# Performance work log

Measured on AMD Instinct MI355X. Metric: run time of the kernel, lower is better.

Reference implementation:

```python
import jax, jax.numpy as jnp
import numpy as np

C, H, W, B = 64, 64, 64, 8

def setup_inputs() -> dict:
    key = jax.random.key(0)
    ks = jax.random.split(key, 6)
    s = 0.05
    return {
        "x": jax.random.normal(ks[0], (B, C, H, W), dtype=jnp.float32),
        "w_cam": jax.random.normal(ks[1], (C, C), dtype=jnp.float32) * s,        # CAM 1x1 conv
        "w_q": jax.random.normal(ks[2], (C // 2, C), dtype=jnp.float32) * s,     # SAM query 1x1 conv
        "w_k": jax.random.normal(ks[3], (C // 2, C), dtype=jnp.float32) * s,     # SAM key 1x1 conv
        "w_v": jax.random.normal(ks[4], (C, C), dtype=jnp.float32) * s,          # SAM value 1x1 conv
        "w_bn": jax.random.normal(ks[5], (C, 2 * C), dtype=jnp.float32) * s,     # bottleneck 1x1 conv 2c->c
    }

def _conv1x1(w, x):
    # w: [O, C], x: [B, C, H, W] -> [B, O, H, W]
    return jnp.einsum('oc,bchw->bohw', w, x)

def reference(x, w_cam, w_q, w_k, w_v, w_bn):
    b, c, h, w = x.shape
    hw = h * w
    # ---- CAM (channel attention) ----
    xc = _conv1x1(w_cam, x).reshape(b, c, hw)            # [b, c, hw]
    energy_c = jnp.einsum('bcn,bdn->bcd', xc, xc)        # [b, c, c]
    attn_c = jax.nn.softmax(energy_c, axis=-1)           # dropout = identity (eval)
    out_c = jnp.einsum('bcd,bdn->bcn', attn_c, x.reshape(b, c, hw)).reshape(b, c, h, w)
    # ---- SAM (spatial attention) ----
    q = _conv1x1(w_q, x).reshape(b, c // 2, hw)          # [b, c/2, hw]
    k = _conv1x1(w_k, x).reshape(b, c // 2, hw)
    v = _conv1x1(w_v, x).reshape(b, c, hw)
    energy_s = jnp.einsum('bcn,bcm->bnm', q, k)          # [b, hw, hw]
    attn_s = jax.nn.softmax(energy_s, axis=-1)           # dropout = identity (eval)
    out_s = jnp.einsum('bcm,bnm->bcn', v, attn_s).reshape(b, c, h, w)
    # ---- fuse: concat -> bottleneck 1x1 conv -> residual ----
    cat = jnp.concatenate([out_c, out_s], axis=1)        # [b, 2c, h, w]
    out = _conv1x1(w_bn, cat)                            # [b, c, h, w]
    return x + out
```

## Files before the change

### kernel.cpp

```cpp
#include <hip/hip_runtime.h>

#define BB 8
#define C 64
#define HW 4096

typedef __attribute__((ext_vector_type(8))) __bf16 bf16x8;
typedef __attribute__((ext_vector_type(16))) float f32x16;
typedef unsigned int uint;
typedef unsigned short ushort;

__device__ __forceinline__ ushort bfb(float f) {
  return __builtin_bit_cast(ushort, (__bf16)f);
}
__device__ __forceinline__ uint pk2(float a, float b) {
  return (uint)bfb(a) | ((uint)bfb(b) << 16);
}
__device__ __forceinline__ uint cvtpk(float a, float b) {
  uint r;
  asm("v_cvt_pk_bf16_f32 %0, %1, %2" : "=v"(r) : "v"(a), "v"(b));
  return r;
}
__device__ __forceinline__ f32x16 mfma_bf16(bf16x8 a, bf16x8 b, f32x16 c) {
  return __builtin_amdgcn_mfma_f32_32x32x16_bf16(a, b, c, 0, 0, 0);
}

__global__ __launch_bounds__(256) void gram_fold_kernel(const float* __restrict__ x,
                                                        float* __restrict__ Gp,
                                                        const float* __restrict__ w_bn,
                                                        const float* __restrict__ w_q,
                                                        const float* __restrict__ w_k,
                                                        const float* __restrict__ w_v,
                                                        char* __restrict__ wall) {
  __shared__ float slots[4][4096];
  const int bxx = blockIdx.x;
  const int t = threadIdx.x;
  if (bxx < 4) {
    const int slot = bxx * 4 + (t >> 6);
    const int ot = slot >> 2, kc = slot & 3;
    const int l = t & 63, lo5 = l & 31, hi = l >> 5;
    float v[8];
    if (ot == 0) {
#pragma unroll
      for (int j = 0; j < 8; ++j)
        v[j] = 1.44269504088896f * w_q[lo5 * 64 + kc * 16 + hi * 8 + j];
    } else if (ot == 1) {
#pragma unroll
      for (int j = 0; j < 8; ++j) v[j] = w_k[lo5 * 64 + kc * 16 + hi * 8 + j];
    } else {
      int c = (ot - 2) * 32 + lo5;
#pragma unroll
      for (int j = 0; j < 8; ++j) {
        int d = kc * 16 + hi * 8 + j;
        float acc = 0.f;
        for (int e = 0; e < 64; ++e) acc += w_bn[c * 128 + 64 + e] * w_v[e * 64 + d];
        v[j] = acc;
      }
    }
    uint4 w;
    w.x = pk2(v[0], v[1]); w.y = pk2(v[2], v[3]);
    w.z = pk2(v[4], v[5]); w.w = pk2(v[6], v[7]);
    *(uint4*)(wall + slot * 1024 + l * 16) = w;
    return;
  }
  const int bx = bxx - 4;
  const int b = bx >> 3, kb = bx & 7;
  const int w = t >> 6, l = t & 63, lo5 = l & 31, hi = l >> 5;
  const int k0 = kb * 512 + w * 128;
  const float* xb = x + (size_t)b * C * HW;
  f32x16 fz;
#pragma unroll
  for (int r = 0; r < 16; ++r) fz[r] = 0.f;
  f32x16 a00 = fz, a01 = fz, a10 = fz, a11 = fz;
#pragma unroll 1
  for (int kc = 0; kc < 8; ++kc) {
    int nb = k0 + kc * 16 + hi * 8;
    const float4* p0 = (const float4*)(xb + (size_t)lo5 * HW + nb);
    const float4* p1 = (const float4*)(xb + (size_t)(32 + lo5) * HW + nb);
    float v0[8], v1[8];
    {
      float4 a = p0[0], bq = p0[1];
      v0[0] = a.x; v0[1] = a.y; v0[2] = a.z; v0[3] = a.w;
      v0[4] = bq.x; v0[5] = bq.y; v0[6] = bq.z; v0[7] = bq.w;
      float4 c = p1[0], d = p1[1];
      v1[0] = c.x; v1[1] = c.y; v1[2] = c.z; v1[3] = c.w;
      v1[4] = d.x; v1[5] = d.y; v1[6] = d.z; v1[7] = d.w;
    }
    uint4 uh0, ul0, uh1, ul1;
    {
      float h[8], e[8];
#pragma unroll
      for (int j = 0; j < 8; ++j) { h[j] = (float)(__bf16)v0[j]; e[j] = v0[j] - h[j]; }
      uh0.x = pk2(h[0], h[1]); uh0.y = pk2(h[2], h[3]); uh0.z = pk2(h[4], h[5]); uh0.w = pk2(h[6], h[7]);
      ul0.x = cvtpk(e[0], e[1]); ul0.y = cvtpk(e[2], e[3]); ul0.z = cvtpk(e[4], e[5]); ul0.w = cvtpk(e[6], e[7]);
#pragma unroll
      for (int j = 0; j < 8; ++j) { h[j] = (float)(__bf16)v1[j]; e[j] = v1[j] - h[j]; }
      uh1.x = pk2(h[0], h[1]); uh1.y = pk2(h[2], h[3]); uh1.z = pk2(h[4], h[5]); uh1.w = pk2(h[6], h[7]);
      ul1.x = cvtpk(e[0], e[1]); ul1.y = cvtpk(e[2], e[3]); ul1.z = cvtpk(e[4], e[5]); ul1.w = cvtpk(e[6], e[7]);
    }
    bf16x8 f0h = __builtin_bit_cast(bf16x8, uh0);
    bf16x8 f0l = __builtin_bit_cast(bf16x8, ul0);
    bf16x8 f1h = __builtin_bit_cast(bf16x8, uh1);
    bf16x8 f1l = __builtin_bit_cast(bf16x8, ul1);
    a00 = mfma_bf16(f0h, f0h, a00); a00 = mfma_bf16(f0h, f0l, a00); a00 = mfma_bf16(f0l, f0h, a00);
    a01 = mfma_bf16(f0h, f1h, a01); a01 = mfma_bf16(f0h, f1l, a01); a01 = mfma_bf16(f0l, f1h, a01);
    a10 = mfma_bf16(f1h, f0h, a10); a10 = mfma_bf16(f1h, f0l, a10); a10 = mfma_bf16(f1l, f0h, a10);
    a11 = mfma_bf16(f1h, f1h, a11); a11 = mfma_bf16(f1h, f1l, a11); a11 = mfma_bf16(f1l, f1h, a11);
  }
#pragma unroll
  for (int r = 0; r < 16; ++r) {
    int row = (r & 3) + 8 * (r >> 2) + 4 * hi;
    slots[w][row * 64 + lo5] = a00[r];
    slots[w][row * 64 + 32 + lo5] = a01[r];
    slots[w][(32 + row) * 64 + lo5] = a10[r];
    slots[w][(32 + row) * 64 + 32 + lo5] = a11[r];
  }
  __syncthreads();
  float* g = Gp + (size_t)(b * 8 + kb) * 4096;
#pragma unroll
  for (int i = 0; i < 16; ++i) {
    int idx = t + i * 256;
    g[idx] = slots[0][idx] + slots[1][idx] + slots[2][idx] + slots[3][idx];
  }
}

__device__ __forceinline__ void cam_body(const float* __restrict__ Gp,
                                         const float* __restrict__ w_cam,
                                         const float* __restrict__ w_bn,
                                         float* __restrict__ m1,
                                         int b, float* buf) {
  const int t = threadIdx.x;
#pragma unroll
  for (int i = 0; i < 16; ++i) {
    int idx = t + i * 256;
    float s = 0.f;
#pragma unroll
    for (int p = 0; p < 8; ++p)
      s += Gp[(size_t)(b * 8 + p) * 4096 + idx];
    buf[idx] = s;
  }
  __syncthreads();
  const int lane = t & 63, rg = (t >> 6) * 16;
  float acc[16];
#pragma unroll
  for (int r = 0; r < 16; ++r) acc[r] = 0.f;
  for (int c = 0; c < 64; ++c) {
    float g = buf[c * 64 + lane];
#pragma unroll
    for (int r = 0; r < 16; ++r) acc[r] += w_cam[(rg + r) * 64 + c] * g;
  }
  __syncthreads();
#pragma unroll
  for (int r = 0; r < 16; ++r) buf[(rg + r) * 64 + lane] = acc[r];
  __syncthreads();
#pragma unroll
  for (int r = 0; r < 16; ++r) acc[r] = 0.f;
  for (int d = 0; d < 64; ++d) {
    float wl = w_cam[lane * 64 + d];
#pragma unroll
    for (int r = 0; r < 16; ++r) acc[r] += buf[(rg + r) * 64 + d] * wl;
  }
  __syncthreads();
#pragma unroll
  for (int r = 0; r < 16; ++r) buf[(rg + r) * 64 + lane] = acc[r];
  __syncthreads();
  {
    int row = t >> 2, c0 = (t & 3) * 16;
    float v[16];
    float mx = -1e30f;
#pragma unroll
    for (int j = 0; j < 16; ++j) { v[j] = buf[row * 64 + c0 + j]; mx = fmaxf(mx, v[j]); }
    mx = fmaxf(mx, __shfl_xor(mx, 1));
    mx = fmaxf(mx, __shfl_xor(mx, 2));
    float s = 0.f;
#pragma unroll
    for (int j = 0; j < 16; ++j) { v[j] = __expf(v[j] - mx); s += v[j]; }
    s += __shfl_xor(s, 1);
    s += __shfl_xor(s, 2);
    float inv = 1.f / s;
#pragma unroll
    for (int j = 0; j < 16; ++j) buf[row * 64 + c0 + j] = v[j] * inv;
  }
  __syncthreads();
  float a2[16];
#pragma unroll
  for (int dd = 0; dd < 16; ++dd) a2[dd] = 0.f;
  for (int r = 0; r < 64; ++r) {
    float wv = w_bn[lane * 128 + r];
#pragma unroll
    for (int dd = 0; dd < 16; ++dd) a2[dd] += wv * buf[r * 64 + rg + dd];
  }
  float* mb = m1 + (size_t)b * 4096;
#pragma unroll
  for (int dd = 0; dd < 16; ++dd) mb[(rg + dd) * 64 + lane] = a2[dd];
}

__global__ __launch_bounds__(256) void prep_cam_kernel(const float* __restrict__ x,
                                                       const char* __restrict__ wall,
                                                       char* __restrict__ qd2,
                                                       char* __restrict__ kd2,
                                                       char* __restrict__ vpd2,
                                                       const float* __restrict__ Gp,
                                                       const float* __restrict__ w_cam,
                                                       const float* __restrict__ w_bn,
                                                       float* __restrict__ m1) {
  __shared__ float buf[4096];
  const int bxx = blockIdx.x;
  if (bxx < 8) {
    cam_body(Gp, w_cam, w_bn, m1, bxx, buf);
    return;
  }
  const int bx = bxx - 8;
  const int t = threadIdx.x;
  const int w = t >> 6, l = t & 63, lo5 = l & 31, hi = l >> 5;
  const int chunk = bx * 2 + (w & 1);
  const int p2 = w >> 1;
  const int b = chunk >> 7;
  const int c7 = chunk & 127;
  const int n0 = c7 * 32;
  const int tt = c7 >> 1;
  const int n = n0 + lo5;
  const float* xb = x + (size_t)b * C * HW;

  f32x16 fz;
#pragma unroll
  for (int r = 0; r < 16; ++r) fz[r] = 0.f;

  bf16x8 xf[4];
#pragma unroll
  for (int kc = 0; kc < 4; ++kc) {
    float xv[8];
#pragma unroll
    for (int j = 0; j < 8; ++j)
      xv[j] = xb[(size_t)(kc * 16 + hi * 8 + j) * HW + n];
    uint4 u;
    u.x = cvtpk(xv[0], xv[1]); u.y = cvtpk(xv[2], xv[3]);
    u.z = cvtpk(xv[4], xv[5]); u.w = cvtpk(xv[6], xv[7]);
    xf[kc] = __builtin_bit_cast(bf16x8, u);
  }

#pragma unroll
  for (int oo = 0; oo < 2; ++oo) {
    const int ot = p2 * 2 + oo;
    f32x16 acc = fz;
#pragma unroll
    for (int kc = 0; kc < 4; ++kc) {
      bf16x8 wf = *(const bf16x8*)(wall + ((ot << 2) | kc) * 1024 + l * 16);
      acc = (p2 == 0) ? mfma_bf16(wf, xf[kc], acc)
                      : mfma_bf16(xf[kc], wf, acc);
    }
    char* base;
    int estride;
    if (ot == 0) {
      base = qd2 + ((size_t)b * HW + n) * 64 + hi * 8;
      estride = 16;
    } else if (ot == 1) {
      base = kd2 + ((size_t)(b * 64 + tt)) * 4096 + (c7 & 1) * 2048 + lo5 * 16 + hi * 8;
      estride = 512;
    } else {
      base = vpd2 + ((size_t)(b * 64 + tt)) * 8192 + (ot - 2) * 4096 +
             (c7 & 1) * 2048 + lo5 * 16 + hi * 8;
      estride = 512;
    }
    {
      uint2 u0, u1, u2, u3;
      u0.x = cvtpk(acc[0], acc[1]);   u0.y = cvtpk(acc[2], acc[3]);
      u1.x = cvtpk(acc[4], acc[5]);   u1.y = cvtpk(acc[6], acc[7]);
      u2.x = cvtpk(acc[8], acc[9]);   u2.y = cvtpk(acc[10], acc[11]);
      u3.x = cvtpk(acc[12], acc[13]); u3.y = cvtpk(acc[14], acc[15]);
      *(uint2*)(base) = u0;
      *(uint2*)(base + estride) = u1;
      *(uint2*)(base + 2 * estride) = u2;
      *(uint2*)(base + 3 * estride) = u3;
    }
  }
}

__global__ __launch_bounds__(256) void fa_kernel(const char* __restrict__ qd2,
                                                 const char* __restrict__ kd2,
                                                 const char* __restrict__ vpd2,
                                                 char* __restrict__ op,
                                                 float* __restrict__ lp) {
  const int t = threadIdx.x;
  const int l = t & 63, lo5 = l & 31, hi = l >> 5;
  const int wv = t >> 6;
  const int bx = blockIdx.x;
  const int g = (bx & 7) | ((bx >> 8) << 3);
  const int qt = (bx >> 3) & 31;
  const int b = g >> 2, kvs = g & 3;
  const int nq = qt * 128 + wv * 32 + lo5;

  const char* qb = qd2 + ((size_t)b * HW + nq) * 64;
  bf16x8 qf0 = *(const bf16x8*)(qb + hi * 16);
  bf16x8 qf1 = *(const bf16x8*)(qb + 32 + hi * 16);

  f32x16 fz;
#pragma unroll
  for (int r = 0; r < 16; ++r) fz[r] = 0.f;
  f32x16 o0 = fz, o1 = fz, lacc = fz;

  uint4 ow;
  {
    uint ob = (lo5 == 0) ? 0x3F803F80u : 0u;
    ow.x = ob; ow.y = ob; ow.z = ob; ow.w = ob;
  }
  const bf16x8 onesf = __builtin_bit_cast(bf16x8, ow);

  const char* kbase = kd2 + ((size_t)(b * 64 + kvs * 16)) * 4096 + l * 16;
  const char* vbase = vpd2 + ((size_t)(b * 64 + kvs * 16)) * 8192 + l * 16;

  bf16x8 kf0 = *(const bf16x8*)(kbase);
  bf16x8 kf1 = *(const bf16x8*)(kbase + 1024);
  bf16x8 kf2 = *(const bf16x8*)(kbase + 2048);
  bf16x8 kf3 = *(const bf16x8*)(kbase + 3072);

#pragma unroll 1
  for (int i = 0; i < 16; ++i) {
    bf16x8 kn0, kn1, kn2, kn3;
    if (i < 15) {
      const char* kn = kbase + (size_t)(i + 1) * 4096;
      kn0 = *(const bf16x8*)(kn);
      kn1 = *(const bf16x8*)(kn + 1024);
      kn2 = *(const bf16x8*)(kn + 2048);
      kn3 = *(const bf16x8*)(kn + 3072);
    }
    const char* vb = vbase + (size_t)i * 8192;
    bf16x8 vfa[4], vfb[4];
#pragma unroll
    for (int ks = 0; ks < 4; ++ks) {
      vfa[ks] = *(const bf16x8*)(vb + ks * 1024);
      vfb[ks] = *(const bf16x8*)(vb + 4096 + ks * 1024);
    }
    f32x16 s0 = mfma_bf16(kf0, qf0, fz);
    s0 = mfma_bf16(kf1, qf1, s0);
    f32x16 s1 = mfma_bf16(kf2, qf0, fz);
    s1 = mfma_bf16(kf3, qf1, s1);
#pragma unroll
    for (int r = 0; r < 16; ++r) s0[r] = __builtin_amdgcn_exp2f(s0[r]);
#pragma unroll
    for (int r = 0; r < 16; ++r) s1[r] = __builtin_amdgcn_exp2f(s1[r]);
#pragma unroll
    for (int ks = 0; ks < 4; ++ks) {
      const f32x16& pm = (ks < 2) ? s0 : s1;
      const int rb = (ks & 1) * 8;
      uint w0 = cvtpk(pm[rb + 0], pm[rb + 1]);
      uint w1 = cvtpk(pm[rb + 2], pm[rb + 3]);
      uint w2 = cvtpk(pm[rb + 4], pm[rb + 5]);
      uint w3 = cvtpk(pm[rb + 6], pm[rb + 7]);
      uint x0 = __shfl_xor(w0, 32);
      uint x1 = __shfl_xor(w1, 32);
      uint x2 = __shfl_xor(w2, 32);
      uint x3 = __shfl_xor(w3, 32);
      uint4 fw;
      fw.x = hi ? x2 : w0;
      fw.y = hi ? x3 : w1;
      fw.z = hi ? w2 : x0;
      fw.w = hi ? w3 : x1;
      bf16x8 pf = __builtin_bit_cast(bf16x8, fw);
      o0 = mfma_bf16(vfa[ks], pf, o0);
      o1 = mfma_bf16(vfb[ks], pf, o1);
      lacc = mfma_bf16(onesf, pf, lacc);
    }
    kf0 = kn0; kf1 = kn1; kf2 = kn2; kf3 = kn3;
  }

  ushort* opu = (ushort*)op;
  const size_t obase = ((size_t)(b * 64) * 4 + kvs) * HW + nq;
#pragma unroll
  for (int r = 0; r < 16; ++r) {
    int c0 = (r & 3) + 8 * (r >> 2) + 4 * hi;
    opu[obase + (size_t)c0 * 4 * HW] = bfb(o0[r]);
    opu[obase + (size_t)(c0 + 32) * 4 * HW] = bfb(o1[r]);
  }
  if (hi == 0) lp[(size_t)(kvs * 8 + b) * HW + nq] = lacc[0];
}

__global__ __launch_bounds__(256) void final_kernel(const float* __restrict__ x,
                                                    const float* __restrict__ m1,
                                                    const char* __restrict__ op,
                                                    const float* __restrict__ lp,
                                                    float* __restrict__ outp) {
  __shared__ __align__(16) float xt[4096];
  __shared__ __align__(16) float ms[4096];
  const int b = blockIdx.y, tt = blockIdx.x, t = threadIdx.x;
  const float4* xg = (const float4*)(x + (size_t)b * C * HW);
  float4* xt4 = (float4*)xt;
#pragma unroll
  for (int i = 0; i < 4; ++i) {
    int idx = t + i * 256;
    int c = idx >> 4, ng = idx & 15;
    xt4[c * 16 + (ng ^ (c & 15))] = xg[c * 1024 + tt * 16 + ng];
  }
  float4* ms4 = (float4*)ms;
  const float4* mg = (const float4*)(m1 + (size_t)b * 4096);
#pragma unroll
  for (int i = 0; i < 4; ++i) ms4[t + i * 256] = mg[t + i * 256];
  __syncthreads();
  const int n = t & 63, sub = t >> 6;
  const int gn = tt * 64 + n;
  float xr[64];
#pragma unroll
  for (int c = 0; c < 64; ++c)
    xr[c] = xt[c * 64 + (((n >> 2) ^ (c & 15)) << 2) + (n & 3)];
  float lsum = 0.f;
#pragma unroll
  for (int kvs = 0; kvs < 4; ++kvs) lsum += lp[(size_t)(kvs * 8 + b) * HW + gn];
  float linv = 1.f / lsum;
  const ushort* opu = (const ushort*)op;
  float acc[16];
#pragma unroll
  for (int ci = 0; ci < 16; ++ci) {
    int c = sub * 16 + ci;
    float osum = 0.f;
#pragma unroll
    for (int kvs = 0; kvs < 4; ++kvs) {
      ushort u = opu[((size_t)(b * 64 + c) * 4 + kvs) * HW + gn];
      osum += __builtin_bit_cast(float, (uint)u << 16);
    }
    acc[ci] = xr[c] + osum * linv;
  }
  for (int d = 0; d < 64; ++d) {
    float xv = xr[d];
    const float4* mr = (const float4*)(ms + d * 64 + sub * 16);
#pragma unroll
    for (int c4 = 0; c4 < 4; ++c4) {
      float4 mv = mr[c4];
      acc[c4 * 4 + 0] += mv.x * xv;
      acc[c4 * 4 + 1] += mv.y * xv;
      acc[c4 * 4 + 2] += mv.z * xv;
      acc[c4 * 4 + 3] += mv.w * xv;
    }
  }
  float* ob = outp + (size_t)b * C * HW + gn;
#pragma unroll
  for (int ci = 0; ci < 16; ++ci)
    ob[(size_t)(sub * 16 + ci) * HW] = acc[ci];
}

extern "C" void kernel_launch(void* const* d_in, const int* in_sizes, int n_in,
                              void* d_out, int out_size, void* d_ws, size_t ws_size,
                              hipStream_t stream) {
  const float* x     = (const float*)d_in[0];
  const float* w_cam = (const float*)d_in[1];
  const float* w_q   = (const float*)d_in[2];
  const float* w_k   = (const float*)d_in[3];
  const float* w_v   = (const float*)d_in[4];
  const float* w_bn  = (const float*)d_in[5];
  float* out = (float*)d_out;
  char* wsb = (char*)d_ws;

  char*  wall = wsb;
  float* m1   = (float*)(wsb + 16384);
  char*  qd2  = wsb + 147456;
  char*  kd2  = qd2 + 2097152;
  char*  vpd2 = kd2 + 2097152;
  float* lp   = (float*)(vpd2 + 4194304);
  char*  op   = (char*)lp + 524288;
  float* Gp   = (float*)op;

  gram_fold_kernel<<<68, 256, 0, stream>>>(x, Gp, w_bn, w_q, w_k, w_v, wall);
  prep_cam_kernel<<<520, 256, 0, stream>>>(x, wall, qd2, kd2, vpd2, Gp, w_cam, w_bn, m1);
  fa_kernel<<<1024, 256, 0, stream>>>(qd2, kd2, vpd2, op, lp);
  final_kernel<<<dim3(64, BB), 256, 0, stream>>>(x, m1, op, lp, out);
}
```

Baseline: 116.3 us.

## Process two query tiles per wave in attention; split Gram reduction finer

The attention kernel now has each wave handle two 32-row query tiles that share the same K/V fragments. This halves the K/V global loads per query and halves the grid to 512 blocks, in exchange for more accumulator registers and possibly lower occupancy. Separately, the Gram partial kernel now splits each batch across 32 chunks instead of 8, giving 260 blocks instead of 68 so more CUs are busy. The cost is four times as many partial matrices that the CAM stage must sum, which also enlarges the Gp scratch region.

```diff
diff --git a/kernel.cpp b/kernel.cpp
--- a/kernel.cpp
+++ b/kernel.cpp
@@ -63,16 +63,16 @@
     return;
   }
   const int bx = bxx - 4;
-  const int b = bx >> 3, kb = bx & 7;
+  const int b = bx >> 5, kb = bx & 31;
   const int w = t >> 6, l = t & 63, lo5 = l & 31, hi = l >> 5;
-  const int k0 = kb * 512 + w * 128;
+  const int k0 = kb * 128 + w * 32;
   const float* xb = x + (size_t)b * C * HW;
   f32x16 fz;
 #pragma unroll
   for (int r = 0; r < 16; ++r) fz[r] = 0.f;
   f32x16 a00 = fz, a01 = fz, a10 = fz, a11 = fz;
 #pragma unroll 1
-  for (int kc = 0; kc < 8; ++kc) {
+  for (int kc = 0; kc < 2; ++kc) {
     int nb = k0 + kc * 16 + hi * 8;
     const float4* p0 = (const float4*)(xb + (size_t)lo5 * HW + nb);
     const float4* p1 = (const float4*)(xb + (size_t)(32 + lo5) * HW + nb);
@@ -115,7 +115,7 @@
     slots[w][(32 + row) * 64 + 32 + lo5] = a11[r];
   }
   __syncthreads();
-  float* g = Gp + (size_t)(b * 8 + kb) * 4096;
+  float* g = Gp + (size_t)(b * 32 + kb) * 4096;
 #pragma unroll
   for (int i = 0; i < 16; ++i) {
     int idx = t + i * 256;
@@ -134,8 +134,8 @@
     int idx = t + i * 256;
     float s = 0.f;
 #pragma unroll
-    for (int p = 0; p < 8; ++p)
-      s += Gp[(size_t)(b * 8 + p) * 4096 + idx];
+    for (int p = 0; p < 32; ++p)
+      s += Gp[(size_t)(b * 32 + p) * 4096 + idx];
     buf[idx] = s;
   }
   __syncthreads();
@@ -284,19 +284,24 @@
   const int l = t & 63, lo5 = l & 31, hi = l >> 5;
   const int wv = t >> 6;
   const int bx = blockIdx.x;
-  const int g = (bx & 7) | ((bx >> 8) << 3);
-  const int qt = (bx >> 3) & 31;
+  const int g = (bx & 7) | ((bx >> 7) << 3);
+  const int qt = (bx >> 3) & 15;
   const int b = g >> 2, kvs = g & 3;
-  const int nq = qt * 128 + wv * 32 + lo5;
-
-  const char* qb = qd2 + ((size_t)b * HW + nq) * 64;
-  bf16x8 qf0 = *(const bf16x8*)(qb + hi * 16);
-  bf16x8 qf1 = *(const bf16x8*)(qb + 32 + hi * 16);
+  const int nqA = qt * 256 + wv * 64 + lo5;
+  const int nqB = nqA + 32;
+
+  const char* qbA = qd2 + ((size_t)b * HW + nqA) * 64;
+  const char* qbB = qd2 + ((size_t)b * HW + nqB) * 64;
+  bf16x8 qfA0 = *(const bf16x8*)(qbA + hi * 16);
+  bf16x8 qfA1 = *(const bf16x8*)(qbA + 32 + hi * 16);
+  bf16x8 qfB0 = *(const bf16x8*)(qbB + hi * 16);
+  bf16x8 qfB1 = *(const bf16x8*)(qbB + 32 + hi * 16);
 
   f32x16 fz;
 #pragma unroll
   for (int r = 0; r < 16; ++r) fz[r] = 0.f;
-  f32x16 o0 = fz, o1 = fz, lacc = fz;
+  f32x16 oA0 = fz, oA1 = fz, lA = fz;
+  f32x16 oB0 = fz, oB1 = fz, lB = fz;
 
   uint4 ow;
   {
@@ -330,48 +335,80 @@
       vfa[ks] = *(const bf16x8*)(vb + ks * 1024);
       vfb[ks] = *(const bf16x8*)(vb + 4096 + ks * 1024);
     }
-    f32x16 s0 = mfma_bf16(kf0, qf0, fz);
-    s0 = mfma_bf16(kf1, qf1, s0);
-    f32x16 s1 = mfma_bf16(kf2, qf0, fz);
-    s1 = mfma_bf16(kf3, qf1, s1);
-#pragma unroll
-    for (int r = 0; r < 16; ++r) s0[r] = __builtin_amdgcn_exp2f(s0[r]);
-#pragma unroll
-    for (int r = 0; r < 16; ++r) s1[r] = __builtin_amdgcn_exp2f(s1[r]);
+    f32x16 sA0 = mfma_bf16(kf0, qfA0, fz);
+    sA0 = mfma_bf16(kf1, qfA1, sA0);
+    f32x16 sA1 = mfma_bf16(kf2, qfA0, fz);
+    sA1 = mfma_bf16(kf3, qfA1, sA1);
+    f32x16 sB0 = mfma_bf16(kf0, qfB0, fz);
+    sB0 = mfma_bf16(kf1, qfB1, sB0);
+    f32x16 sB1 = mfma_bf16(kf2, qfB0, fz);
+    sB1 = mfma_bf16(kf3, qfB1, sB1);
+#pragma unroll
+    for (int r = 0; r < 16; ++r) sA0[r] = __builtin_amdgcn_exp2f(sA0[r]);
+#pragma unroll
+    for (int r = 0; r < 16; ++r) sA1[r] = __builtin_amdgcn_exp2f(sA1[r]);
+#pragma unroll
+    for (int r = 0; r < 16; ++r) sB0[r] = __builtin_amdgcn_exp2f(sB0[r]);
+#pragma unroll
+    for (int r = 0; r < 16; ++r) sB1[r] = __builtin_amdgcn_exp2f(sB1[r]);
 #pragma unroll
     for (int ks = 0; ks < 4; ++ks) {
-      const f32x16& pm = (ks < 2) ? s0 : s1;
+      const f32x16& pmA = (ks < 2) ? sA0 : sA1;
+      const f32x16& pmB = (ks < 2) ? sB0 : sB1;
       const int rb = (ks & 1) * 8;
-      uint w0 = cvtpk(pm[rb + 0], pm[rb + 1]);
-      uint w1 = cvtpk(pm[rb + 2], pm[rb + 3]);
-      uint w2 = cvtpk(pm[rb + 4], pm[rb + 5]);
-      uint w3 = cvtpk(pm[rb + 6], pm[rb + 7]);
-      uint x0 = __shfl_xor(w0, 32);
-      uint x1 = __shfl_xor(w1, 32);
-      uint x2 = __shfl_xor(w2, 32);
-      uint x3 = __shfl_xor(w3, 32);
-      uint4 fw;
-      fw.x = hi ? x2 : w0;
-      fw.y = hi ? x3 : w1;
-      fw.z = hi ? w2 : x0;
-      fw.w = hi ? w3 : x1;
-      bf16x8 pf = __builtin_bit_cast(bf16x8, fw);
-      o0 = mfma_bf16(vfa[ks], pf, o0);
-      o1 = mfma_bf16(vfb[ks], pf, o1);
-      lacc = mfma_bf16(onesf, pf, lacc);
+      uint wA0 = cvtpk(pmA[rb + 0], pmA[rb + 1]);
+      uint wA1 = cvtpk(pmA[rb + 2], pmA[rb + 3]);
+      uint wA2 = cvtpk(pmA[rb + 4], pmA[rb + 5]);
+      uint wA3 = cvtpk(pmA[rb + 6], pmA[rb + 7]);
+      uint xA0 = __shfl_xor(wA0, 32);
+      uint xA1 = __shfl_xor(wA1, 32);
+      uint xA2 = __shfl_xor(wA2, 32);
+      uint xA3 = __shfl_xor(wA3, 32);
+      uint4 fwA;
+      fwA.x = hi ? xA2 : wA0;
+      fwA.y = hi ? xA3 : wA1;
+      fwA.z = hi ? wA2 : xA0;
+      fwA.w = hi ? wA3 : xA1;
+      bf16x8 pfA = __builtin_bit_cast(bf16x8, fwA);
+      oA0 = mfma_bf16(vfa[ks], pfA, oA0);
+      oA1 = mfma_bf16(vfb[ks], pfA, oA1);
+      lA = mfma_bf16(onesf, pfA, lA);
+      uint wB0 = cvtpk(pmB[rb + 0], pmB[rb + 1]);
+      uint wB1 = cvtpk(pmB[rb + 2], pmB[rb + 3]);
+      uint wB2 = cvtpk(pmB[rb + 4], pmB[rb + 5]);
+      uint wB3 = cvtpk(pmB[rb + 6], pmB[rb + 7]);
+      uint xB0 = __shfl_xor(wB0, 32);
+      uint xB1 = __shfl_xor(wB1, 32);
+      uint xB2 = __shfl_xor(wB2, 32);
+      uint xB3 = __shfl_xor(wB3, 32);
+      uint4 fwB;
+      fwB.x = hi ? xB2 : wB0;
+      fwB.y = hi ? xB3 : wB1;
+      fwB.z = hi ? wB2 : xB0;
+      fwB.w = hi ? wB3 : xB1;
+      bf16x8 pfB = __builtin_bit_cast(bf16x8, fwB);
+      oB0 = mfma_bf16(vfa[ks], pfB, oB0);
+      oB1 = mfma_bf16(vfb[ks], pfB, oB1);
+      lB = mfma_bf16(onesf, pfB, lB);
     }
     kf0 = kn0; kf1 = kn1; kf2 = kn2; kf3 = kn3;
   }
 
   ushort* opu = (ushort*)op;
-  const size_t obase = ((size_t)(b * 64) * 4 + kvs) * HW + nq;
+  const size_t obaseA = ((size_t)(b * 64) * 4 + kvs) * HW + nqA;
+  const size_t obaseB = obaseA + 32;
 #pragma unroll
   for (int r = 0; r < 16; ++r) {
     int c0 = (r & 3) + 8 * (r >> 2) + 4 * hi;
-    opu[obase + (size_t)c0 * 4 * HW] = bfb(o0[r]);
-    opu[obase + (size_t)(c0 + 32) * 4 * HW] = bfb(o1[r]);
-  }
-  if (hi == 0) lp[(size_t)(kvs * 8 + b) * HW + nq] = lacc[0];
+    opu[obaseA + (size_t)c0 * 4 * HW] = bfb(oA0[r]);
+    opu[obaseA + (size_t)(c0 + 32) * 4 * HW] = bfb(oA1[r]);
+    opu[obaseB + (size_t)c0 * 4 * HW] = bfb(oB0[r]);
+    opu[obaseB + (size_t)(c0 + 32) * 4 * HW] = bfb(oB1[r]);
+  }
+  if (hi == 0) {
+    lp[(size_t)(kvs * 8 + b) * HW + nqA] = lA[0];
+    lp[(size_t)(kvs * 8 + b) * HW + nqB] = lB[0];
+  }
 }
 
 __global__ __launch_bounds__(256) void final_kernel(const float* __restrict__ x,
@@ -457,8 +494,8 @@
   char*  op   = (char*)lp + 524288;
   float* Gp   = (float*)op;
 
-  gram_fold_kernel<<<68, 256, 0, stream>>>(x, Gp, w_bn, w_q, w_k, w_v, wall);
+  gram_fold_kernel<<<260, 256, 0, stream>>>(x, Gp, w_bn, w_q, w_k, w_v, wall);
   prep_cam_kernel<<<520, 256, 0, stream>>>(x, wall, qd2, kd2, vpd2, Gp, w_cam, w_bn, m1);
-  fa_kernel<<<1024, 256, 0, stream>>>(qd2, kd2, vpd2, op, lp);
+  fa_kernel<<<512, 256, 0, stream>>>(qd2, kd2, vpd2, op, lp);
   final_kernel<<<dim3(64, BB), 256, 0, stream>>>(x, m1, op, lp, out);
 }
```

Measured after the change: 129.3 us. 1.11x slower.
